# Kernel optimization log

Measured on AMD Instinct MI355X. Metric: run time of the kernel, lower is better.

The kernel has to match this reference:

```python
import jax, jax.numpy as jnp
import numpy as np

D_MODEL = 512
N_HEAD = 8
D_HEAD = D_MODEL // N_HEAD


def _linear(x, W, b):
    return x @ W + b


def setup_inputs() -> dict:
    key = jax.random.key(0)
    ks = jax.random.split(key, 20)
    B, N, D = 8, 1024, D_MODEL
    H = D // 2
    s = 1.0 / np.sqrt(D)
    s2 = 1.0 / np.sqrt(H)
    inp = {
        'query': jax.random.normal(ks[0], (B, N, D), jnp.float32),
        'key_in': jax.random.normal(ks[1], (B, N, D), jnp.float32),
        'value': jax.random.normal(ks[2], (B, N, D), jnp.float32),
        'Wq': jax.random.normal(ks[3], (D, D), jnp.float32) * s,
        'bq': jnp.zeros((D,), jnp.float32),
        'Wk': jax.random.normal(ks[4], (D, D), jnp.float32) * s,
        'bk': jnp.zeros((D,), jnp.float32),
        'Wv': jax.random.normal(ks[5], (D, D), jnp.float32) * s,
        'bv': jnp.zeros((D,), jnp.float32),
        'Wo': jax.random.normal(ks[6], (D, D), jnp.float32) * s,
        'bo': jnp.zeros((D,), jnp.float32),
        'Ws1': jax.random.normal(ks[7], (D, H), jnp.float32) * s,
        'bs1': jnp.zeros((H,), jnp.float32),
        'Ws2': jax.random.normal(ks[8], (H, D), jnp.float32) * s2,
        'bs2': jnp.zeros((D,), jnp.float32),
        'Wc1': jax.random.normal(ks[9], (D, H), jnp.float32) * s,
        'bc1': jnp.zeros((H,), jnp.float32),
        'Wc2': jax.random.normal(ks[10], (H, D), jnp.float32) * s2,
        'bc2': jnp.zeros((D,), jnp.float32),
    }
    return inp


def reference(query, key_in, value, Wq, bq, Wk, bk, Wv, bv, Wo, bo,
              Ws1, bs1, Ws2, bs2, Wc1, bc1, Wc2, bc2):
    B, N, D = query.shape
    H, Dh = N_HEAD, D_HEAD

    def split_heads(x):  # [b, n, h*d] -> [b, h, n, d]
        return x.reshape(B, N, H, Dh).transpose(0, 2, 1, 3)

    q = split_heads(_linear(query, Wq, bq))
    k = split_heads(_linear(key_in, Wk, bk))
    vv = _linear(value, Wv, bv)  # [b, n, d] == rearrange(v,'b h n d->b n (h d)')

    # spatial gating: Linear-ReLU-Linear-Sigmoid on w_v(value)
    sw = jax.nn.sigmoid(_linear(jax.nn.relu(_linear(vv, Ws1, bs1)), Ws2, bs2))
    v_spatial = split_heads(vv * sw)

    # channel gating: MLP on mean-over-seq profile, broadcast back to seq
    prof = value.mean(axis=1, keepdims=True)  # [b, 1, d]
    cw = jax.nn.sigmoid(_linear(jax.nn.relu(_linear(prof, Wc1, bc1)), Wc2, bc2))
    v_channel = split_heads(_linear(value * cw, Wv, bv))

    v_dual = v_spatial + v_channel

    scores = jnp.einsum('bhqd,bhkd->bhqk', q, k) / np.sqrt(Dh).astype(np.float32)
    attn = jax.nn.softmax(scores, axis=-1)
    out = jnp.einsum('bhqk,bhkd->bhqd', attn, v_dual)
    out = out.transpose(0, 2, 1, 3).reshape(B, N, D)
    return _linear(out, Wo, bo)  # dropout is identity in eval mode
```

## Files before the change

### kernel.cpp

```cpp
#include <hip/hip_runtime.h>

typedef unsigned short u16t;
typedef __bf16  bf8   __attribute__((ext_vector_type(8)));
typedef float   f32x4 __attribute__((ext_vector_type(4)));
typedef unsigned short us4 __attribute__((ext_vector_type(4)));

#define DEV __device__ __forceinline__

DEV float bf2f(u16t u) { union { unsigned u; float f; } x; x.u = ((unsigned)u) << 16; return x.f; }
DEV u16t  f2bf(float f) {
    union { float f; unsigned u; } x; x.f = f;
    unsigned r = x.u + 0x7FFFu + ((x.u >> 16) & 1u);
    return (u16t)(r >> 16);
}
DEV uint4 pack8(const float* v) {
    uint4 r;
    r.x = (unsigned)f2bf(v[0]) | ((unsigned)f2bf(v[1]) << 16);
    r.y = (unsigned)f2bf(v[2]) | ((unsigned)f2bf(v[3]) << 16);
    r.z = (unsigned)f2bf(v[4]) | ((unsigned)f2bf(v[5]) << 16);
    r.w = (unsigned)f2bf(v[6]) | ((unsigned)f2bf(v[7]) << 16);
    return r;
}
DEV void gll16(const void* g, void* l) {
    __builtin_amdgcn_global_load_lds(
        (const __attribute__((address_space(1))) unsigned*)g,
        (__attribute__((address_space(3))) unsigned*)l, 16, 0, 0);
}

#define DMODEL 512
#define SEQ    1024
#define NBATCH 8

__global__ __launch_bounds__(256) void fill_sentinel(float* out, int n)
{
    int i = blockIdx.x * 256 + threadIdx.x;
    if (i < n) out[i] = 100.f;
}

__global__ __launch_bounds__(256) void cvt_value(const float* v, u16t* Vi)
{
    size_t i = ((size_t)blockIdx.x * 256 + threadIdx.x) * 8;
    float4 a = *(const float4*)(v + i), b = *(const float4*)(v + i + 4);
    float o[8] = {a.x, a.y, a.z, a.w, b.x, b.y, b.z, b.w};
    *(uint4*)&Vi[i] = pack8(o);
}

__global__ __launch_bounds__(256) void transpose6(
    const float* s0, const float* s1, const float* s2, const float* s3,
    const float* s4, const float* s5,
    u16t* d0, u16t* d1, u16t* d2, u16t* d3, u16t* d4, u16t* d5)
{
    int z = blockIdx.z;
    const float* S; u16t* D; int R, C;
    switch (z) {
        case 0: S = s0; D = d0; R = 512; C = 512; break;
        case 1: S = s1; D = d1; R = 512; C = 512; break;
        case 2: S = s2; D = d2; R = 512; C = 512; break;
        case 3: S = s3; D = d3; R = 512; C = 512; break;
        case 4: S = s4; D = d4; R = 512; C = 256; break;
        default:S = s5; D = d5; R = 256; C = 512; break;
    }
    int c0 = blockIdx.x * 32, r0 = blockIdx.y * 32;
    if (c0 >= C || r0 >= R) return;
    __shared__ u16t tile[32][33];
    int tx = threadIdx.x & 31, ty = threadIdx.x >> 5;
#pragma unroll
    for (int p = 0; p < 4; ++p) {
        int r = ty + p * 8;
        tile[r][tx] = f2bf(S[(size_t)(r0 + r) * C + c0 + tx]);
    }
    __syncthreads();
#pragma unroll
    for (int p = 0; p < 4; ++p) {
        int r = ty + p * 8;
        D[(size_t)(c0 + r) * R + r0 + tx] = tile[tx][r];
    }
}

__global__ __launch_bounds__(256) void colmean(const u16t* Vi, float* prof)
{
    int b = blockIdx.y, z = blockIdx.z;
    int d = blockIdx.x * 256 + threadIdx.x;
    const u16t* p = Vi + (size_t)b * SEQ * DMODEL + (size_t)z * 64 * DMODEL + d;
    float s = 0.f;
#pragma unroll 8
    for (int n = 0; n < 64; ++n) s += bf2f(p[(size_t)n * DMODEL]);
    atomicAdd(&prof[b * DMODEL + d], s * (1.f / 1024.f));
}

__global__ __launch_bounds__(256) void cmlp(const float* prof,
                                            const float* Wc1, const float* bc1,
                                            const float* Wc2, const float* bc2,
                                            u16t* cw)
{
    int b = blockIdx.x, t = threadIdx.x;
    __shared__ float pf[512];
    __shared__ float hf[256];
    pf[t]       = prof[b * 512 + t];
    pf[t + 256] = prof[b * 512 + t + 256];
    __syncthreads();
    float s = bc1[t];
    for (int k = 0; k < 512; ++k) s += pf[k] * Wc1[(size_t)k * 256 + t];
    hf[t] = fmaxf(s, 0.f);
    __syncthreads();
#pragma unroll
    for (int o = 0; o < 2; ++o) {
        int d = t + o * 256;
        float s2 = bc2[d];
        for (int k = 0; k < 256; ++k) s2 += hf[k] * Wc2[(size_t)k * 512 + d];
        cw[b * 512 + d] = f2bf(1.f / (1.f + __expf(-s2)));
    }
}

__global__ __launch_bounds__(256) void scale_wv(const u16t* WvT, const u16t* cw,
                                                u16t* WvTs)
{
    int b = blockIdx.y;
    int idx = blockIdx.x * 2048 + threadIdx.x * 8;
    int k = idx & 511;
    uint4 wv = *(const uint4*)&WvT[idx];
    uint4 cu = *(const uint4*)&cw[b * 512 + k];
    const u16t* wp = (const u16t*)&wv;
    const u16t* cp = (const u16t*)&cu;
    float o[8];
#pragma unroll
    for (int q = 0; q < 8; ++q) o[q] = bf2f(wp[q]) * bf2f(cp[q]);
    *(uint4*)&WvTs[(size_t)b * 262144 + idx] = pack8(o);
}

__global__ __launch_bounds__(256) void gemm_bt(
    const void* A0, const void* A1, const void* A2, const void* A3,
    const u16t* W0, const u16t* W1, const u16t* W2, const u16t* W3,
    const float* B0, const float* B1, const float* B2, const float* B3,
    void* C0, void* C1, void* C2, void* C3,
    int N, int K, int mode,
    const u16t* VVp, u16t* VdTp,
    int araw, int tmask, int outf32, int wbmask)
{
    int z = blockIdx.z;
    const void* A  = (z == 0) ? A0 : (z == 1) ? A1 : (z == 2) ? A2 : A3;
    const u16t* W  = (z == 0) ? W0 : (z == 1) ? W1 : (z == 2) ? W2 : W3;
    const float* Bi = (z == 0) ? B0 : (z == 1) ? B1 : (z == 2) ? B2 : B3;
    void*       C  = (z == 0) ? C0 : (z == 1) ? C1 : (z == 2) ? C2 : C3;

    int af32   = (araw >> z) & 1;
    int tstore = (tmask >> z) & 1;

    int tid = threadIdx.x;
    int w = tid >> 6, lane = tid & 63, quad = lane >> 4, l16 = lane & 15;
    int wrow = w >> 1, wcol = w & 1;
    int m0 = blockIdx.y * 128, n0 = blockIdx.x * 128;
    int bb = m0 >> 10;
    if ((wbmask >> z) & 1) W += (size_t)bb * 262144;

    __shared__ __align__(16) u16t As[128 * 32];
    __shared__ __align__(16) u16t Bs[128 * 32];

    f32x4 zero = {0.f, 0.f, 0.f, 0.f};
    f32x4 acc[4][4];
#pragma unroll
    for (int i = 0; i < 4; ++i)
#pragma unroll
        for (int j = 0; j < 4; ++j) acc[i][j] = zero;

    for (int k0 = 0; k0 < K; k0 += 32) {
        __syncthreads();
        if (af32) {
            const float* Af = (const float*)A;
            int r_ = tid >> 2, g_ = tid & 3;
#pragma unroll
            for (int p = 0; p < 2; ++p) {
                int r = r_ + p * 64;
                int gs = (g_ ^ (r & 3)) * 8;
                const float* src = Af + (size_t)(m0 + r) * K + k0 + gs;
                float4 a = *(const float4*)src;
                float4 b = *(const float4*)(src + 4);
                float v[8] = {a.x, a.y, a.z, a.w, b.x, b.y, b.z, b.w};
                *(uint4*)&As[r * 32 + g_ * 8] = pack8(v);
            }
#pragma unroll
            for (int p = 0; p < 2; ++p) {
                int ci = p * 256 + tid;
                int r = ci >> 2, g = ci & 3;
                int gs = (g ^ (r & 3)) * 8;
                gll16(&W[(size_t)(n0 + r) * K + k0 + gs], &Bs[(size_t)(p * 256 + w * 64) * 8]);
            }
        } else {
            const u16t* Ab = (const u16t*)A;
#pragma unroll
            for (int p = 0; p < 2; ++p) {
                int ci = p * 256 + tid;
                int r = ci >> 2, g = ci & 3;
                int gs = (g ^ (r & 3)) * 8;
                gll16(&Ab[(size_t)(m0 + r) * K + k0 + gs], &As[(size_t)(p * 256 + w * 64) * 8]);
                gll16(&W[(size_t)(n0 + r) * K + k0 + gs],  &Bs[(size_t)(p * 256 + w * 64) * 8]);
            }
        }
        __syncthreads();
        bf8 af[4], bfr[4];
#pragma unroll
        for (int i = 0; i < 4; ++i) {
            int sq = (quad ^ (l16 & 3)) * 8;
            af[i]  = *(const bf8*)&As[(wrow * 64 + i * 16 + l16) * 32 + sq];
            bfr[i] = *(const bf8*)&Bs[(wcol * 64 + i * 16 + l16) * 32 + sq];
        }
#pragma unroll
        for (int i = 0; i < 4; ++i)
#pragma unroll
            for (int j = 0; j < 4; ++j)
                acc[i][j] = __builtin_amdgcn_mfma_f32_16x16x32_bf16(af[i], bfr[j], acc[i][j], 0, 0, 0);
    }

#pragma unroll
    for (int i = 0; i < 4; ++i) {
        int grow0 = m0 + wrow * 64 + i * 16 + quad * 4;
#pragma unroll
        for (int j = 0; j < 4; ++j) {
            int gcol = n0 + wcol * 64 + j * 16 + l16;
            float bias = Bi[gcol];
            if (mode == 2) {
                int h = gcol >> 6, dh = gcol & 63;
                int b_ = grow0 >> 10, n_ = grow0 & 1023;
                size_t tbase = (size_t)((b_ * 8 + h) * 64 + dh) * 1024 + n_;
                us4 vc = *(const us4*)&VdTp[tbase];
                us4 pk;
#pragma unroll
                for (int r = 0; r < 4; ++r) {
                    float s = acc[i][j][r] + bias;
                    float sw = 1.f / (1.f + __expf(-s));
                    float vvv = bf2f(VVp[(size_t)(grow0 + r) * DMODEL + gcol]);
                    pk[r] = f2bf(vvv * sw + bf2f(vc[r]));
                }
                *(us4*)&VdTp[tbase] = pk;
            } else if (tstore) {
                int h = gcol >> 6, dh = gcol & 63;
                int b_ = grow0 >> 10, n_ = grow0 & 1023;
                us4 pk;
#pragma unroll
                for (int r = 0; r < 4; ++r) pk[r] = f2bf(acc[i][j][r] + bias);
                *(us4*)&((u16t*)C)[(size_t)((b_ * 8 + h) * 64 + dh) * 1024 + n_] = pk;
            } else if (outf32) {
#pragma unroll
                for (int r = 0; r < 4; ++r)
                    ((float*)C)[(size_t)(grow0 + r) * N + gcol] = acc[i][j][r] + bias;
            } else {
#pragma unroll
                for (int r = 0; r < 4; ++r) {
                    float v = acc[i][j][r] + bias;
                    if (mode == 1) v = fmaxf(v, 0.f);
                    ((u16t*)C)[(size_t)(grow0 + r) * N + gcol] = f2bf(v);
                }
            }
        }
    }
}

__global__ __launch_bounds__(256) void attn(const u16t* Q, const u16t* Km,
                                            const u16t* VdT, u16t* Oa)
{
    __shared__ __align__(16) u16t Qs[64 * 64];
    __shared__ __align__(16) u16t Ks[64 * 64];
    __shared__ __align__(16) u16t Vs[64 * 64];
    __shared__ __align__(16) u16t Ps[64 * 64];

    int qt = blockIdx.x, bh = blockIdx.y;
    int b = bh >> 3, h = bh & 7;
    int tid = threadIdx.x;
    int w = tid >> 6, lane = tid & 63, quad = lane >> 4, l16 = lane & 15;
    int l7 = l16 & 7;

    const u16t* Qp = Q   + ((size_t)(b * SEQ + qt * 64)) * DMODEL + h * 64;
    const u16t* Kp = Km  + ((size_t)(b * SEQ)) * DMODEL + h * 64;
    const u16t* Vp = VdT + ((size_t)(b * 8 + h)) * 64 * SEQ;

#pragma unroll
    for (int p = 0; p < 2; ++p) {
        int ci = p * 256 + tid;
        int r = ci >> 3, g = ci & 7;
        int gs = (g ^ (r & 7)) * 8;
        gll16(&Qp[(size_t)r * DMODEL + gs], &Qs[(size_t)(p * 256 + w * 64) * 8]);
    }

    f32x4 zero = {0.f, 0.f, 0.f, 0.f};
    f32x4 oacc[4];
    float l_run[4];
#pragma unroll
    for (int r = 0; r < 4; ++r) { l_run[r] = 0.f; oacc[r] = zero; }

    for (int kt = 0; kt < 16; ++kt) {
        __syncthreads();
#pragma unroll
        for (int p = 0; p < 2; ++p) {
            int ci = p * 256 + tid;
            int r = ci >> 3, g = ci & 7;
            int gs = (g ^ (r & 7)) * 8;
            gll16(&Kp[(size_t)(kt * 64 + r) * DMODEL + gs], &Ks[(size_t)(p * 256 + w * 64) * 8]);
            gll16(&Vp[(size_t)r * SEQ + kt * 64 + gs],      &Vs[(size_t)(p * 256 + w * 64) * 8]);
        }
        __syncthreads();

        f32x4 sacc[4];
#pragma unroll
        for (int j = 0; j < 4; ++j) sacc[j] = zero;
#pragma unroll
        for (int ks = 0; ks < 2; ++ks) {
            int sG = ((ks * 4 + quad) ^ l7) * 8;
            bf8 aq = *(const bf8*)&Qs[(w * 16 + l16) * 64 + sG];
            bf8 bk[4];
#pragma unroll
            for (int j = 0; j < 4; ++j)
                bk[j] = *(const bf8*)&Ks[(j * 16 + l16) * 64 + sG];
#pragma unroll
            for (int j = 0; j < 4; ++j)
                sacc[j] = __builtin_amdgcn_mfma_f32_16x16x32_bf16(aq, bk[j], sacc[j], 0, 0, 0);
        }

#pragma unroll
        for (int r4 = 0; r4 < 4; ++r4) {
            float rsum = 0.f;
            int prow = w * 16 + quad * 4 + r4;
            int pr7 = prow & 7;
#pragma unroll
            for (int j = 0; j < 4; ++j) {
                float p = __expf(fmaf(sacc[j][r4], 0.125f, -4.f));
                rsum += p;
                int G = j * 2 + (l16 >> 3);
                Ps[prow * 64 + ((G ^ pr7) * 8) + l7] = f2bf(p);
            }
#pragma unroll
            for (int d = 1; d < 16; d <<= 1) rsum += __shfl_xor(rsum, d);
            l_run[r4] += rsum;
        }

#pragma unroll
        for (int kk = 0; kk < 2; ++kk) {
            int sG = ((kk * 4 + quad) ^ l7) * 8;
            bf8 ap = *(const bf8*)&Ps[(w * 16 + l16) * 64 + sG];
            bf8 bvf[4];
#pragma unroll
            for (int j = 0; j < 4; ++j)
                bvf[j] = *(const bf8*)&Vs[(j * 16 + l16) * 64 + sG];
#pragma unroll
            for (int j = 0; j < 4; ++j)
                oacc[j] = __builtin_amdgcn_mfma_f32_16x16x32_bf16(ap, bvf[j], oacc[j], 0, 0, 0);
        }
    }

#pragma unroll
    for (int j = 0; j < 4; ++j) {
#pragma unroll
        for (int r4 = 0; r4 < 4; ++r4) {
            int rq = qt * 64 + w * 16 + quad * 4 + r4;
            float v = oacc[j][r4] / l_run[r4];
            Oa[((size_t)(b * SEQ + rq)) * DMODEL + h * 64 + j * 16 + l16] = f2bf(v);
        }
    }
}

extern "C" void kernel_launch(void* const* d_in, const int* in_sizes, int n_in,
                              void* d_out, int out_size, void* d_ws, size_t ws_size,
                              hipStream_t stream)
{
    const float* query  = (const float*)d_in[0];
    const float* key_in = (const float*)d_in[1];
    const float* value  = (const float*)d_in[2];
    const float* Wq  = (const float*)d_in[3];  const float* bq  = (const float*)d_in[4];
    const float* Wk  = (const float*)d_in[5];  const float* bk  = (const float*)d_in[6];
    const float* Wv  = (const float*)d_in[7];  const float* bv  = (const float*)d_in[8];
    const float* Wo  = (const float*)d_in[9];  const float* bo  = (const float*)d_in[10];
    const float* Ws1 = (const float*)d_in[11]; const float* bs1 = (const float*)d_in[12];
    const float* Ws2 = (const float*)d_in[13]; const float* bs2 = (const float*)d_in[14];
    const float* Wc1 = (const float*)d_in[15]; const float* bc1 = (const float*)d_in[16];
    const float* Wc2 = (const float*)d_in[17]; const float* bc2 = (const float*)d_in[18];
    float* out = (float*)d_out;

    u16t* ws = (u16t*)d_ws;
    u16t* WqT  = ws + 0;
    u16t* WkT  = ws + 262144;
    u16t* WvT  = ws + 524288;
    u16t* WoT  = ws + 786432;
    u16t* Ws1T = ws + 1048576;
    u16t* Ws2T = ws + 1179648;
    u16t* WvTs = ws + 1310720;
    u16t* Vi   = ws + 3407872;
    u16t* Qm   = ws + 7602176;
    u16t* Kmm  = ws + 11796480;
    u16t* VV   = ws + 15990784;
    u16t* VdT  = ws + 20185088;
    u16t* cw   = ws + 24379392;
    float* prof = (float*)(ws + 24383488);
    u16t* H1 = Vi;
    u16t* Oa = VV;

    const size_t NEED_BYTES = 24391680ull * 2ull;
    if (ws_size < NEED_BYTES) {
        fill_sentinel<<<(out_size + 255) / 256, 256, 0, stream>>>(out, out_size);
        return;
    }

    hipMemsetAsync((void*)prof, 0, NBATCH * DMODEL * sizeof(float), stream);

    cvt_value<<<2048, 256, 0, stream>>>(value, Vi);
    transpose6<<<dim3(16, 16, 6), 256, 0, stream>>>(Wq, Wk, Wv, Wo, Ws1, Ws2,
                                                    WqT, WkT, WvT, WoT, Ws1T, Ws2T);
    colmean<<<dim3(2, 8, 16), 256, 0, stream>>>(Vi, prof);
    cmlp<<<8, 256, 0, stream>>>(prof, Wc1, bc1, Wc2, bc2, cw);
    scale_wv<<<dim3(128, 8), 256, 0, stream>>>(WvT, cw, WvTs);

    gemm_bt<<<dim3(4, 64, 4), 256, 0, stream>>>(
        query, key_in, Vi, Vi,
        WqT, WkT, WvT, WvTs,
        bq, bk, bv, bv,
        Qm, Kmm, VV, VdT,
        512, 512, 0, nullptr, VdT,
        0x3, 0x8, 0, 0x8);

    gemm_bt<<<dim3(2, 64, 1), 256, 0, stream>>>(
        VV, VV, VV, VV, Ws1T, Ws1T, Ws1T, Ws1T, bs1, bs1, bs1, bs1,
        H1, H1, H1, H1, 256, 512, 1, nullptr, nullptr, 0, 0, 0, 0);

    gemm_bt<<<dim3(4, 64, 1), 256, 0, stream>>>(
        H1, H1, H1, H1, Ws2T, Ws2T, Ws2T, Ws2T, bs2, bs2, bs2, bs2,
        Qm, Qm, Qm, Qm,
        512, 256, 2, VV, VdT, 0, 0, 0, 0);

    attn<<<dim3(16, 64), 256, 0, stream>>>(Qm, Kmm, VdT, Oa);

    gemm_bt<<<dim3(4, 64, 1), 256, 0, stream>>>(
        Oa, Oa, Oa, Oa, WoT, WoT, WoT, WoT, bo, bo, bo, bo,
        out, out, out, out, 512, 512, 0, nullptr, nullptr,
        0, 0, 1, 0);
}
```

Baseline: 300.2 us.

## Replace 128x128 GEMM tiles with 64-row tiles and templated column width

The shared GEMM kernel moves from 128x128 output tiles (each wave computing 4x4 MFMA blocks) to 64-row by NT*16-column tiles, where each wave owns 16 rows and NT column blocks. This multiplies the number of workgroups so the small GEMMs (8192 rows) fill all compute units better. The cost is lower data reuse per loaded tile, more global and LDS traffic per FLOP, and fewer MFMAs between barriers.

```diff
diff --git a/kernel.cpp b/kernel.cpp
--- a/kernel.cpp
+++ b/kernel.cpp
@@ -128,7 +128,8 @@
     *(uint4*)&WvTs[(size_t)b * 262144 + idx] = pack8(o);
 }
 
-__global__ __launch_bounds__(256) void gemm_bt(
+template<int NT>
+__global__ __launch_bounds__(256) void gemm64(
     const void* A0, const void* A1, const void* A2, const void* A3,
     const u16t* W0, const u16t* W1, const u16t* W2, const u16t* W3,
     const float* B0, const float* B1, const float* B2, const float* B3,
@@ -148,108 +149,89 @@
 
     int tid = threadIdx.x;
     int w = tid >> 6, lane = tid & 63, quad = lane >> 4, l16 = lane & 15;
-    int wrow = w >> 1, wcol = w & 1;
-    int m0 = blockIdx.y * 128, n0 = blockIdx.x * 128;
+    int m0 = blockIdx.x * 64, n0 = blockIdx.y * (NT * 16);
     int bb = m0 >> 10;
     if ((wbmask >> z) & 1) W += (size_t)bb * 262144;
 
-    __shared__ __align__(16) u16t As[128 * 32];
-    __shared__ __align__(16) u16t Bs[128 * 32];
+    __shared__ __align__(16) u16t As[64 * 32];
+    __shared__ __align__(16) u16t Bs[NT * 16 * 32];
 
     f32x4 zero = {0.f, 0.f, 0.f, 0.f};
-    f32x4 acc[4][4];
-#pragma unroll
-    for (int i = 0; i < 4; ++i)
-#pragma unroll
-        for (int j = 0; j < 4; ++j) acc[i][j] = zero;
+    f32x4 acc[NT];
+#pragma unroll
+    for (int j = 0; j < NT; ++j) acc[j] = zero;
 
     for (int k0 = 0; k0 < K; k0 += 32) {
         __syncthreads();
-        if (af32) {
-            const float* Af = (const float*)A;
-            int r_ = tid >> 2, g_ = tid & 3;
-#pragma unroll
-            for (int p = 0; p < 2; ++p) {
-                int r = r_ + p * 64;
-                int gs = (g_ ^ (r & 3)) * 8;
-                const float* src = Af + (size_t)(m0 + r) * K + k0 + gs;
+        {
+            int r = tid >> 2, g = tid & 3;
+            int gs = (g ^ (r & 3)) * 8;
+            if (af32) {
+                const float* src = (const float*)A + (size_t)(m0 + r) * K + k0 + gs;
                 float4 a = *(const float4*)src;
                 float4 b = *(const float4*)(src + 4);
                 float v[8] = {a.x, a.y, a.z, a.w, b.x, b.y, b.z, b.w};
-                *(uint4*)&As[r * 32 + g_ * 8] = pack8(v);
+                *(uint4*)&As[r * 32 + g * 8] = pack8(v);
+            } else {
+                gll16(&((const u16t*)A)[(size_t)(m0 + r) * K + k0 + gs],
+                      &As[(size_t)(w * 64) * 8]);
             }
-#pragma unroll
-            for (int p = 0; p < 2; ++p) {
-                int ci = p * 256 + tid;
-                int r = ci >> 2, g = ci & 3;
-                int gs = (g ^ (r & 3)) * 8;
-                gll16(&W[(size_t)(n0 + r) * K + k0 + gs], &Bs[(size_t)(p * 256 + w * 64) * 8]);
+        }
+#pragma unroll
+        for (int p = 0; p < NT / 4; ++p) {
+            int ci = p * 256 + tid;
+            int r = ci >> 2, g = ci & 3;
+            int gs = (g ^ (r & 3)) * 8;
+            gll16(&W[(size_t)(n0 + r) * K + k0 + gs], &Bs[(size_t)(p * 256 + w * 64) * 8]);
+        }
+        __syncthreads();
+        int sq = (quad ^ (l16 & 3)) * 8;
+        bf8 aq = *(const bf8*)&As[(w * 16 + l16) * 32 + sq];
+        bf8 bk[NT];
+#pragma unroll
+        for (int j = 0; j < NT; ++j)
+            bk[j] = *(const bf8*)&Bs[(j * 16 + l16) * 32 + sq];
+#pragma unroll
+        for (int j = 0; j < NT; ++j)
+            acc[j] = __builtin_amdgcn_mfma_f32_16x16x32_bf16(aq, bk[j], acc[j], 0, 0, 0);
+    }
+
+    int grow0 = m0 + w * 16 + quad * 4;
+#pragma unroll
+    for (int j = 0; j < NT; ++j) {
+        int gcol = n0 + j * 16 + l16;
+        float bias = Bi[gcol];
+        if (mode == 2) {
+            int h = gcol >> 6, dh = gcol & 63;
+            int b_ = grow0 >> 10, n_ = grow0 & 1023;
+            size_t tbase = (size_t)((b_ * 8 + h) * 64 + dh) * 1024 + n_;
+            us4 vc = *(const us4*)&VdTp[tbase];
+            us4 pk;
+#pragma unroll
+            for (int r = 0; r < 4; ++r) {
+                float s = acc[j][r] + bias;
+                float sw = 1.f / (1.f + __expf(-s));
+                float vvv = bf2f(VVp[(size_t)(grow0 + r) * DMODEL + gcol]);
+                pk[r] = f2bf(vvv * sw + bf2f(vc[r]));
             }
+            *(us4*)&VdTp[tbase] = pk;
+        } else if (tstore) {
+            int h = gcol >> 6, dh = gcol & 63;
+            int b_ = grow0 >> 10, n_ = grow0 & 1023;
+            us4 pk;
+#pragma unroll
+            for (int r = 0; r < 4; ++r) pk[r] = f2bf(acc[j][r] + bias);
+            *(us4*)&((u16t*)C)[(size_t)((b_ * 8 + h) * 64 + dh) * 1024 + n_] = pk;
+        } else if (outf32) {
+#pragma unroll
+            for (int r = 0; r < 4; ++r)
+                ((float*)C)[(size_t)(grow0 + r) * N + gcol] = acc[j][r] + bias;
         } else {
-            const u16t* Ab = (const u16t*)A;
-#pragma unroll
-            for (int p = 0; p < 2; ++p) {
-                int ci = p * 256 + tid;
-                int r = ci >> 2, g = ci & 3;
-                int gs = (g ^ (r & 3)) * 8;
-                gll16(&Ab[(size_t)(m0 + r) * K + k0 + gs], &As[(size_t)(p * 256 + w * 64) * 8]);
-                gll16(&W[(size_t)(n0 + r) * K + k0 + gs],  &Bs[(size_t)(p * 256 + w * 64) * 8]);
-            }
-        }
-        __syncthreads();
-        bf8 af[4], bfr[4];
-#pragma unroll
-        for (int i = 0; i < 4; ++i) {
-            int sq = (quad ^ (l16 & 3)) * 8;
-            af[i]  = *(const bf8*)&As[(wrow * 64 + i * 16 + l16) * 32 + sq];
-            bfr[i] = *(const bf8*)&Bs[(wcol * 64 + i * 16 + l16) * 32 + sq];
-        }
-#pragma unroll
-        for (int i = 0; i < 4; ++i)
-#pragma unroll
-            for (int j = 0; j < 4; ++j)
-                acc[i][j] = __builtin_amdgcn_mfma_f32_16x16x32_bf16(af[i], bfr[j], acc[i][j], 0, 0, 0);
-    }
-
-#pragma unroll
-    for (int i = 0; i < 4; ++i) {
-        int grow0 = m0 + wrow * 64 + i * 16 + quad * 4;
-#pragma unroll
-        for (int j = 0; j < 4; ++j) {
-            int gcol = n0 + wcol * 64 + j * 16 + l16;
-            float bias = Bi[gcol];
-            if (mode == 2) {
-                int h = gcol >> 6, dh = gcol & 63;
-                int b_ = grow0 >> 10, n_ = grow0 & 1023;
-                size_t tbase = (size_t)((b_ * 8 + h) * 64 + dh) * 1024 + n_;
-                us4 vc = *(const us4*)&VdTp[tbase];
-                us4 pk;
-#pragma unroll
-                for (int r = 0; r < 4; ++r) {
-                    float s = acc[i][j][r] + bias;
-                    float sw = 1.f / (1.f + __expf(-s));
-                    float vvv = bf2f(VVp[(size_t)(grow0 + r) * DMODEL + gcol]);
-                    pk[r] = f2bf(vvv * sw + bf2f(vc[r]));
-                }
-                *(us4*)&VdTp[tbase] = pk;
-            } else if (tstore) {
-                int h = gcol >> 6, dh = gcol & 63;
-                int b_ = grow0 >> 10, n_ = grow0 & 1023;
-                us4 pk;
-#pragma unroll
-                for (int r = 0; r < 4; ++r) pk[r] = f2bf(acc[i][j][r] + bias);
-                *(us4*)&((u16t*)C)[(size_t)((b_ * 8 + h) * 64 + dh) * 1024 + n_] = pk;
-            } else if (outf32) {
-#pragma unroll
-                for (int r = 0; r < 4; ++r)
-                    ((float*)C)[(size_t)(grow0 + r) * N + gcol] = acc[i][j][r] + bias;
-            } else {
-#pragma unroll
-                for (int r = 0; r < 4; ++r) {
-                    float v = acc[i][j][r] + bias;
-                    if (mode == 1) v = fmaxf(v, 0.f);
-                    ((u16t*)C)[(size_t)(grow0 + r) * N + gcol] = f2bf(v);
-                }
+#pragma unroll
+            for (int r = 0; r < 4; ++r) {
+                float v = acc[j][r] + bias;
+                if (mode == 1) v = fmaxf(v, 0.f);
+                ((u16t*)C)[(size_t)(grow0 + r) * N + gcol] = f2bf(v);
             }
         }
     }
@@ -407,7 +389,7 @@
     cmlp<<<8, 256, 0, stream>>>(prof, Wc1, bc1, Wc2, bc2, cw);
     scale_wv<<<dim3(128, 8), 256, 0, stream>>>(WvT, cw, WvTs);
 
-    gemm_bt<<<dim3(4, 64, 4), 256, 0, stream>>>(
+    gemm64<8><<<dim3(128, 4, 4), 256, 0, stream>>>(
         query, key_in, Vi, Vi,
         WqT, WkT, WvT, WvTs,
         bq, bk, bv, bv,
@@ -415,18 +397,18 @@
         512, 512, 0, nullptr, VdT,
         0x3, 0x8, 0, 0x8);
 
-    gemm_bt<<<dim3(2, 64, 1), 256, 0, stream>>>(
+    gemm64<4><<<dim3(128, 4, 1), 256, 0, stream>>>(
         VV, VV, VV, VV, Ws1T, Ws1T, Ws1T, Ws1T, bs1, bs1, bs1, bs1,
         H1, H1, H1, H1, 256, 512, 1, nullptr, nullptr, 0, 0, 0, 0);
 
-    gemm_bt<<<dim3(4, 64, 1), 256, 0, stream>>>(
+    gemm64<8><<<dim3(128, 4, 1), 256, 0, stream>>>(
         H1, H1, H1, H1, Ws2T, Ws2T, Ws2T, Ws2T, bs2, bs2, bs2, bs2,
         Qm, Qm, Qm, Qm,
         512, 256, 2, VV, VdT, 0, 0, 0, 0);
 
     attn<<<dim3(16, 64), 256, 0, stream>>>(Qm, Kmm, VdT, Oa);
 
-    gemm_bt<<<dim3(4, 64, 1), 256, 0, stream>>>(
+    gemm64<8><<<dim3(128, 4, 1), 256, 0, stream>>>(
         Oa, Oa, Oa, Oa, WoT, WoT, WoT, WoT, bo, bo, bo, bo,
         out, out, out, out, 512, 512, 0, nullptr, nullptr,
         0, 0, 1, 0);
```

After: 285.8 us. 1.05x faster.
